# Kernel tuning notes

Measured on AMD Instinct MI355X. Metric: run time of the kernel, lower is better.

## Reference

```python
import jax, jax.numpy as jnp
import numpy as np

B, N, K, E, D, L, LM = 4, 5000, 4, 80000, 512, 6, 3
EPS_MSG = 1e-7   # GENConv message eps
EPS_SM = 1e-16   # PyG scatter-softmax eps
EPS_BN = 1e-5    # BatchNorm eps (eval: running mean=0, var=1)
EPS_LN = 1e-5


def setup_inputs() -> dict:
    key = jax.random.key(0)
    ks = jax.random.split(key, 12)
    s = 0.04  # weight scale for stability
    return {
        "x_idx": jax.random.randint(ks[0], (B, N, K), 0, 25, dtype=jnp.int32),
        "edge_index": jax.random.randint(ks[1], (2, E), 0, N, dtype=jnp.int32),
        "edge_weight": jax.random.uniform(ks[2], (E,), dtype=jnp.float32),
        "node_emb": jax.random.normal(ks[3], (25, D), dtype=jnp.float32),
        "W1": jax.random.normal(ks[4], (L, D, 2 * D), dtype=jnp.float32) * s,
        "b1": jnp.zeros((L, 2 * D), jnp.float32),
        "g1": jnp.ones((L, 2 * D), jnp.float32),
        "be1": jnp.zeros((L, 2 * D), jnp.float32),
        "W2": jax.random.normal(ks[5], (L, 2 * D, D), dtype=jnp.float32) * s,
        "b2": jnp.zeros((L, D), jnp.float32),
        "ln_g": jnp.ones((D,), jnp.float32),
        "ln_b": jnp.zeros((D,), jnp.float32),
        "Wm": jax.random.normal(ks[6], (LM, D, D), dtype=jnp.float32) * s,
        "bm": jnp.zeros((LM, D), jnp.float32),
        "Wout": jax.random.normal(ks[7], (D, 1), dtype=jnp.float32) * s,
        "bout": jnp.zeros((1,), jnp.float32),
    }


def _gen_conv(x, src, dst, edge_weight, W1, b1, g1, be1, W2, b2):
    # x: [B,N,D]; GENConv(aggr='softmax', t=1, num_layers=2, norm='batch' in eval)
    x_j = x[:, src, :]                                            # [B,E,D] gather
    msg = jax.nn.relu(x_j + edge_weight[None, :, None]) + EPS_MSG # [B,E,D]

    def seg_softmax_agg(m):  # m: [E,D] -> [N,D]
        mx = jax.ops.segment_max(m, dst, num_segments=N)          # [N,D]
        ex = jnp.exp(m - mx[dst])
        den = jax.ops.segment_sum(ex, dst, num_segments=N)
        alpha = ex / (den[dst] + EPS_SM)
        return jax.ops.segment_sum(m * alpha, dst, num_segments=N)

    agg = jax.vmap(seg_softmax_agg)(msg)                          # [B,N,D]
    out = agg + x                                                 # residual with x_dst
    h = out @ W1 + b1                                             # [B,N,2D]
    h = h / jnp.sqrt(1.0 + EPS_BN) * g1 + be1                     # BN eval (mean=0, var=1)
    h = jax.nn.relu(h)
    return h @ W2 + b2                                            # [B,N,D]


def reference(x_idx, edge_index, edge_weight, node_emb, W1, b1, g1, be1, W2, b2,
              ln_g, ln_b, Wm, bm, Wout, bout):
    src, dst = edge_index[0], edge_index[1]
    x = node_emb[x_idx].sum(axis=2)                               # [B,N,D]
    for l in range(W1.shape[0]):
        x = _gen_conv(x, src, dst, edge_weight,
                      W1[l], b1[l], g1[l], be1[l], W2[l], b2[l])
        x = jax.nn.relu(x)                                        # EncoderLayer relu (dropout=id in eval)
    mu = x.mean(axis=-1, keepdims=True)
    var = jnp.mean(jnp.square(x - mu), axis=-1, keepdims=True)
    h = (x - mu) * jax.lax.rsqrt(var + EPS_LN) * ln_g + ln_b      # LayerNorm
    for l in range(Wm.shape[0]):
        h = jax.nn.gelu(h @ Wm[l] + bm[l], approximate=False)
    out = h @ Wout + bout                                         # [B,N,1]
    return out.mean(axis=1)                                       # [B,1]
```

## Files before the change

kernel.cpp:

```cpp
#include <hip/hip_runtime.h>
#include <hip/hip_fp16.h>

#define BB 4
#define NN 5000
#define KK 4
#define EE 80000
#define DD 512
#define LL 6
#define LMM 3

typedef _Float16 f16x8 __attribute__((ext_vector_type(8)));
typedef _Float16 f16x4 __attribute__((ext_vector_type(4)));
typedef _Float16 f16x2 __attribute__((ext_vector_type(2)));
typedef float f32x4 __attribute__((ext_vector_type(4)));

__device__ __forceinline__ void async_copy16(_Float16* lds, const _Float16* g) {
    __builtin_amdgcn_global_load_lds((const __attribute__((address_space(1))) void*)g,
                                     (__attribute__((address_space(3))) void*)lds,
                                     16, 0, 0);
}

__global__ void zero_int2(int* a, int* b, int n) {
    int i = blockIdx.x * blockDim.x + threadIdx.x;
    if (i < n) { a[i] = 0; b[i] = 0; }
}

__global__ void count_deg(const int* __restrict__ dst, int* __restrict__ deg) {
    int e = blockIdx.x * blockDim.x + threadIdx.x;
    if (e < EE) atomicAdd(&deg[dst[e]], 1);
}

__global__ __launch_bounds__(1024) void scan_off(const int* __restrict__ deg, int* __restrict__ off) {
    __shared__ int s[1024];
    const int n = NN, tot = NN + 1;
    const int per = (tot + 1023) / 1024;
    int tid = threadIdx.x;
    int start = tid * per;
    int loc[8];
    int sum = 0;
    for (int i = 0; i < per; i++) {
        int idx = start + i;
        int v = (idx < n) ? deg[idx] : 0;
        loc[i] = sum; sum += v;
    }
    s[tid] = sum; __syncthreads();
    for (int o = 1; o < 1024; o <<= 1) {
        int v = (tid >= o) ? s[tid - o] : 0;
        __syncthreads();
        s[tid] += v;
        __syncthreads();
    }
    int base = (tid > 0) ? s[tid - 1] : 0;
    for (int i = 0; i < per; i++) {
        int idx = start + i;
        if (idx < tot) off[idx] = base + loc[i];
    }
}

__global__ void scatter_edges(const int* __restrict__ src, const int* __restrict__ dst,
                              const float* __restrict__ ew, const int* __restrict__ off,
                              int* __restrict__ cursor, int* __restrict__ srcs, float* __restrict__ wss) {
    int e = blockIdx.x * blockDim.x + threadIdx.x;
    if (e >= EE) return;
    int d = dst[e];
    int p = atomicAdd(&cursor[d], 1);
    int idx = off[d] + p;
    srcs[idx] = src[e];
    wss[idx] = ew[e];
}

__global__ __launch_bounds__(256) void embed_kernel(const int* __restrict__ x_idx,
                                                    const float* __restrict__ emb,
                                                    _Float16* __restrict__ x) {
    int row = blockIdx.x;
    int d = threadIdx.x * 2;
    int4 iv = *reinterpret_cast<const int4*>(x_idx + (size_t)row * 4);
    float2 a = *reinterpret_cast<const float2*>(emb + (size_t)iv.x * DD + d);
    float2 b = *reinterpret_cast<const float2*>(emb + (size_t)iv.y * DD + d);
    float2 c = *reinterpret_cast<const float2*>(emb + (size_t)iv.z * DD + d);
    float2 e = *reinterpret_cast<const float2*>(emb + (size_t)iv.w * DD + d);
    f16x2 v;
    v[0] = (_Float16)(a.x + b.x + c.x + e.x);
    v[1] = (_Float16)(a.y + b.y + c.y + e.y);
    *reinterpret_cast<f16x2*>(x + (size_t)row * DD + d) = v;
}

__global__ __launch_bounds__(128) void conv_kernel(const _Float16* __restrict__ x,
                                                   const int* __restrict__ srcs,
                                                   const float* __restrict__ wss,
                                                   const int* __restrict__ off,
                                                   _Float16* __restrict__ t) {
    int n = blockIdx.x, b = blockIdx.y, tid = threadIdx.x;
    const _Float16* xb = x + (size_t)b * NN * DD;
    int e0 = off[n], e1 = off[n + 1];
    __shared__ int   ss[64];
    __shared__ float sw[64];
    int d0 = tid * 4;
    float S0 = 0.f, S1 = 0.f, S2 = 0.f, S3 = 0.f;
    float Z0 = 0.f, Z1 = 0.f, Z2 = 0.f, Z3 = 0.f;
    for (int base = e0; base < e1; base += 64) {
        int cnt = min(64, e1 - base);
        if (tid < cnt) { ss[tid] = srcs[base + tid]; sw[tid] = wss[base + tid]; }
        __syncthreads();
        for (int j = 0; j < cnt; j++) {
            f16x4 xv = *reinterpret_cast<const f16x4*>(xb + (size_t)ss[j] * DD + d0);
            float w = sw[j];
            float m0 = fmaxf((float)xv[0] + w, 0.f) + 1e-7f;
            float m1 = fmaxf((float)xv[1] + w, 0.f) + 1e-7f;
            float m2 = fmaxf((float)xv[2] + w, 0.f) + 1e-7f;
            float m3 = fmaxf((float)xv[3] + w, 0.f) + 1e-7f;
            float p0 = __expf(m0), p1 = __expf(m1), p2 = __expf(m2), p3 = __expf(m3);
            S0 += p0; Z0 = fmaf(m0, p0, Z0);
            S1 += p1; Z1 = fmaf(m1, p1, Z1);
            S2 += p2; Z2 = fmaf(m2, p2, Z2);
            S3 += p3; Z3 = fmaf(m3, p3, Z3);
        }
        __syncthreads();
    }
    f16x4 xn = *reinterpret_cast<const f16x4*>(xb + (size_t)n * DD + d0);
    f16x4 o;
    o[0] = (_Float16)(Z0 / (S0 + 1e-16f) + (float)xn[0]);
    o[1] = (_Float16)(Z1 / (S1 + 1e-16f) + (float)xn[1]);
    o[2] = (_Float16)(Z2 / (S2 + 1e-16f) + (float)xn[2]);
    o[3] = (_Float16)(Z3 / (S3 + 1e-16f) + (float)xn[3]);
    *reinterpret_cast<f16x4*>(t + ((size_t)b * NN + n) * DD + d0) = o;
}

__global__ void transpose_f32_f16(const float* __restrict__ W, _Float16* __restrict__ Wt,
                                  int K, int Nc) {
    __shared__ float tile[32][33];
    size_t loff = (size_t)blockIdx.z * K * Nc;
    int n0 = blockIdx.x * 32, k0 = blockIdx.y * 32;
    int tx = threadIdx.x, ty = threadIdx.y;
    for (int i = 0; i < 32; i += 8)
        tile[ty + i][tx] = W[loff + (size_t)(k0 + ty + i) * Nc + n0 + tx];
    __syncthreads();
    for (int i = 0; i < 32; i += 8)
        Wt[loff + (size_t)(n0 + ty + i) * K + k0 + tx] = (_Float16)tile[tx][ty + i];
}

template <int MODE>
__global__ __launch_bounds__(256) void gemm_kernel(const _Float16* __restrict__ A,
                                                   const _Float16* __restrict__ Bt,
                                                   const float* __restrict__ bias,
                                                   const float* __restrict__ g,
                                                   const float* __restrict__ be,
                                                   _Float16* __restrict__ Cout,
                                                   int M, int N, int K, int nt) {
    constexpr int BM = 128, BN = 128, BK = 32;
    constexpr int BUF = (BM + BN) * BK;
    __shared__ __align__(16) _Float16 smem[2 * BUF];
    int tid = threadIdx.x;
    int bid = blockIdx.x;
    int m0 = (bid / nt) * BM, n0 = (bid % nt) * BN;
    int lane = tid & 63, wave = tid >> 6;
    int wm = (wave & 1) * 64, wn = (wave >> 1) * 64;
    int l16 = lane & 15, quad = lane >> 4;
    int r0 = tid >> 2, c0 = (tid & 3) * 8;
    int r1 = (tid + 256) >> 2, c1 = ((tid + 256) & 3) * 8;
    const _Float16* pa0 = A + (size_t)min(m0 + r0, M - 1) * K + c0;
    const _Float16* pa1 = A + (size_t)min(m0 + r1, M - 1) * K + c1;
    const _Float16* pb0 = Bt + (size_t)(n0 + r0) * K + c0;
    const _Float16* pb1 = Bt + (size_t)(n0 + r1) * K + c1;
    int la0 = tid * 8, la1 = (tid + 256) * 8;
    int lb0 = BM * BK + la0, lb1 = BM * BK + la1;

    f32x4 acc[4][4] = {};
    async_copy16(smem + la0, pa0);
    async_copy16(smem + la1, pa1);
    async_copy16(smem + lb0, pb0);
    async_copy16(smem + lb1, pb1);
    int buf = 0;
    for (int k0 = 0; k0 < K; k0 += BK, buf ^= BUF) {
        __syncthreads();
        int kn = k0 + BK;
        int nb = buf ^ BUF;
        if (kn < K) {
            async_copy16(smem + nb + la0, pa0 + kn);
            async_copy16(smem + nb + la1, pa1 + kn);
            async_copy16(smem + nb + lb0, pb0 + kn);
            async_copy16(smem + nb + lb1, pb1 + kn);
        }
        f16x8 af[4], bf[4];
#pragma unroll
        for (int i = 0; i < 4; i++)
            af[i] = *reinterpret_cast<const f16x8*>(&smem[buf + (wm + i * 16 + l16) * BK + quad * 8]);
#pragma unroll
        for (int j = 0; j < 4; j++)
            bf[j] = *reinterpret_cast<const f16x8*>(&smem[buf + BM * BK + (wn + j * 16 + l16) * BK + quad * 8]);
#pragma unroll
        for (int i = 0; i < 4; i++)
#pragma unroll
            for (int j = 0; j < 4; j++)
                acc[i][j] = __builtin_amdgcn_mfma_f32_16x16x32_f16(af[i], bf[j], acc[i][j], 0, 0, 0);
    }
    __syncthreads();
    const float invs = rsqrtf(1.0f + 1e-5f);
    _Float16* Ct = smem;
#pragma unroll
    for (int p = 0; p < 2; p++) {
        if ((wave >> 1) == p) {
#pragma unroll
            for (int i = 0; i < 4; i++) {
#pragma unroll
                for (int j = 0; j < 4; j++) {
                    int col = n0 + wn + j * 16 + l16;
#pragma unroll
                    for (int r = 0; r < 4; r++) {
                        float v = acc[i][j][r] + bias[col];
                        if (MODE == 0) {
                            v = fmaxf(v * (g[col] * invs) + be[col], 0.f);
                        } else if (MODE == 1) {
                            v = fmaxf(v, 0.f);
                        } else {
                            v = 0.5f * v * (1.0f + erff(v * 0.70710678118654752f));
                        }
                        Ct[(wm + i * 16 + quad * 4 + r) * 64 + j * 16 + l16] = (_Float16)v;
                    }
                }
            }
        }
        __syncthreads();
#pragma unroll
        for (int k = 0; k < 4; k++) {
            int ch = tid + 256 * k;
            int row = ch >> 3, cc = (ch & 7) * 8;
            int grow = m0 + row;
            if (grow < M)
                *reinterpret_cast<f16x8*>(Cout + (size_t)grow * N + n0 + p * 64 + cc) =
                    *reinterpret_cast<const f16x8*>(&Ct[row * 64 + cc]);
        }
        __syncthreads();
    }
}

__device__ __forceinline__ float block_sum_256(float v, volatile float* sbuf) {
    __syncthreads();
    for (int s = 32; s; s >>= 1) v += __shfl_down(v, s);
    int wv = threadIdx.x >> 6, ln = threadIdx.x & 63;
    if (ln == 0) sbuf[wv] = v;
    __syncthreads();
    if (threadIdx.x == 0) sbuf[4] = sbuf[0] + sbuf[1] + sbuf[2] + sbuf[3];
    __syncthreads();
    return sbuf[4];
}

__global__ __launch_bounds__(256) void ln_kernel(const _Float16* __restrict__ x,
                                                 const float* __restrict__ lg,
                                                 const float* __restrict__ lb,
                                                 _Float16* __restrict__ t) {
    __shared__ float sbuf[5];
    size_t row = blockIdx.x;
    int d = threadIdx.x * 2;
    f16x2 xv = *reinterpret_cast<const f16x2*>(x + row * DD + d);
    float v0 = (float)xv[0], v1 = (float)xv[1];
    float mu = block_sum_256(v0 + v1, sbuf) * (1.0f / DD);
    float d0 = v0 - mu, d1 = v1 - mu;
    float var = block_sum_256(d0 * d0 + d1 * d1, sbuf) * (1.0f / DD);
    float rs = rsqrtf(var + 1e-5f);
    f16x2 o;
    o[0] = (_Float16)(d0 * rs * lg[d] + lb[d]);
    o[1] = (_Float16)(d1 * rs * lg[d + 1] + lb[d + 1]);
    *reinterpret_cast<f16x2*>(t + row * DD + d) = o;
}

__global__ void init_out(float* out, const float* __restrict__ bout) {
    if (threadIdx.x < BB) out[threadIdx.x] = bout[0];
}

__global__ __launch_bounds__(256) void final_reduce(const _Float16* __restrict__ h,
                                                    const float* __restrict__ wout,
                                                    float* __restrict__ out) {
    int b = blockIdx.y;
    const _Float16* hb = h + (size_t)b * NN * DD;
    int lane = threadIdx.x & 63, wave = threadIdx.x >> 6;
    float wv[8];
#pragma unroll
    for (int j = 0; j < 8; j++) wv[j] = wout[lane * 8 + j];
    float acc = 0.f;
    for (int n = blockIdx.x * 4 + wave; n < NN; n += gridDim.x * 4) {
        f16x8 hv = *reinterpret_cast<const f16x8*>(hb + (size_t)n * DD + lane * 8);
#pragma unroll
        for (int j = 0; j < 8; j++) acc += (float)hv[j] * wv[j];
    }
    for (int s = 32; s; s >>= 1) acc += __shfl_down(acc, s);
    __shared__ float sb[4];
    if (lane == 0) sb[wave] = acc;
    __syncthreads();
    if (threadIdx.x == 0) atomicAdd(&out[b], (sb[0] + sb[1] + sb[2] + sb[3]) * (1.0f / NN));
}

extern "C" void kernel_launch(void* const* d_in, const int* in_sizes, int n_in,
                              void* d_out, int out_size, void* d_ws, size_t ws_size,
                              hipStream_t stream) {
    const int*   x_idx = (const int*)d_in[0];
    const int*   eidx  = (const int*)d_in[1];
    const float* ew    = (const float*)d_in[2];
    const float* emb   = (const float*)d_in[3];
    const float* W1    = (const float*)d_in[4];
    const float* b1    = (const float*)d_in[5];
    const float* g1    = (const float*)d_in[6];
    const float* be1   = (const float*)d_in[7];
    const float* W2    = (const float*)d_in[8];
    const float* b2    = (const float*)d_in[9];
    const float* lng   = (const float*)d_in[10];
    const float* lnb   = (const float*)d_in[11];
    const float* Wm    = (const float*)d_in[12];
    const float* bm    = (const float*)d_in[13];
    const float* Wout  = (const float*)d_in[14];
    const float* bout  = (const float*)d_in[15];
    float* out = (float*)d_out;

    char* w = (char*)d_ws;
    size_t o = 0;
    auto alloc = [&](size_t bytes) -> void* {
        void* p = w + o;
        o = (o + bytes + 255) & ~(size_t)255;
        return p;
    };
    _Float16*  x    = (_Float16*)alloc((size_t)BB * NN * DD * 2);
    _Float16*  t    = (_Float16*)alloc((size_t)BB * NN * DD * 2);
    _Float16*  h    = (_Float16*)alloc((size_t)BB * NN * 2 * DD * 2);
    _Float16*  W1t  = (_Float16*)alloc((size_t)LL * 2 * DD * DD * 2);
    _Float16*  W2t  = (_Float16*)alloc((size_t)LL * DD * 2 * DD * 2);
    _Float16*  Wmt  = (_Float16*)alloc((size_t)LMM * DD * DD * 2);
    int*    deg    = (int*)alloc((size_t)NN * 4);
    int*    offs   = (int*)alloc((size_t)(NN + 1) * 4);
    int*    cursor = (int*)alloc((size_t)NN * 4);
    int*    srcs   = (int*)alloc((size_t)EE * 4);
    float*  wss    = (float*)alloc((size_t)EE * 4);

    const int* src = eidx;
    const int* dst = eidx + EE;

    zero_int2<<<(NN + 255) / 256, 256, 0, stream>>>(deg, cursor, NN);
    count_deg<<<(EE + 255) / 256, 256, 0, stream>>>(dst, deg);
    scan_off<<<1, 1024, 0, stream>>>(deg, offs);
    scatter_edges<<<(EE + 255) / 256, 256, 0, stream>>>(src, dst, ew, offs, cursor, srcs, wss);
    embed_kernel<<<BB * NN, 256, 0, stream>>>(x_idx, emb, x);

    transpose_f32_f16<<<dim3(2 * DD / 32, DD / 32, LL), dim3(32, 8), 0, stream>>>(W1, W1t, DD, 2 * DD);
    transpose_f32_f16<<<dim3(DD / 32, 2 * DD / 32, LL), dim3(32, 8), 0, stream>>>(W2, W2t, 2 * DD, DD);
    transpose_f32_f16<<<dim3(DD / 32, DD / 32, LMM), dim3(32, 8), 0, stream>>>(Wm, Wmt, DD, DD);

    const int M = BB * NN;
    const int mt = (M + 127) / 128;
    for (int l = 0; l < LL; l++) {
        conv_kernel<<<dim3(NN, BB), 128, 0, stream>>>(x, srcs, wss, offs, t);
        gemm_kernel<0><<<mt * 8, 256, 0, stream>>>(
            t, W1t + (size_t)l * 2 * DD * DD, b1 + (size_t)l * 2 * DD,
            g1 + (size_t)l * 2 * DD, be1 + (size_t)l * 2 * DD, h, M, 2 * DD, DD, 8);
        gemm_kernel<1><<<mt * 4, 256, 0, stream>>>(
            h, W2t + (size_t)l * DD * 2 * DD, b2 + (size_t)l * DD,
            nullptr, nullptr, x, M, DD, 2 * DD, 4);
    }
    ln_kernel<<<M, 256, 0, stream>>>(x, lng, lnb, t);
    gemm_kernel<2><<<mt * 4, 256, 0, stream>>>(
        t, Wmt, bm, nullptr, nullptr, h, M, DD, DD, 4);
    gemm_kernel<2><<<mt * 4, 256, 0, stream>>>(
        h, Wmt + (size_t)DD * DD, bm + DD, nullptr, nullptr, t, M, DD, DD, 4);
    gemm_kernel<2><<<mt * 4, 256, 0, stream>>>(
        t, Wmt + (size_t)2 * DD * DD, bm + 2 * DD, nullptr, nullptr, h, M, DD, DD, 4);
    init_out<<<1, 64, 0, stream>>>(out, bout);
    final_reduce<<<dim3(32, BB), 256, 0, stream>>>(h, Wout, out);
}
```

Baseline: 1.002 ms.

## Use wave-per-node conv, swizzle GEMM LDS, and XCD-aware tile mapping

The message-aggregation kernel now assigns one 64-lane wave per destination node, with each lane handling 8 features. This drops block-wide barriers and widens gathers to 16-byte loads. The GEMM applies an XOR swizzle to LDS column chunks to reduce bank conflicts on fragment reads. It also remaps block IDs so consecutive row tiles land on the same XCD for L2 reuse of A/B, padding the row-tile count to a multiple of 8. The padding adds a few redundant tiles, and the epsilon handling in the softmax is rearranged algebraically.

```diff
diff --git a/kernel.cpp b/kernel.cpp
--- a/kernel.cpp
+++ b/kernel.cpp
@@ -10,7 +10,6 @@
 #define LMM 3
 
 typedef _Float16 f16x8 __attribute__((ext_vector_type(8)));
-typedef _Float16 f16x4 __attribute__((ext_vector_type(4)));
 typedef _Float16 f16x2 __attribute__((ext_vector_type(2)));
 typedef float f32x4 __attribute__((ext_vector_type(4)));
 
@@ -90,40 +89,39 @@
                                                    const float* __restrict__ wss,
                                                    const int* __restrict__ off,
                                                    _Float16* __restrict__ t) {
-    int n = blockIdx.x, b = blockIdx.y, tid = threadIdx.x;
+    int b = blockIdx.x;
+    int wave = threadIdx.x >> 6, lane = threadIdx.x & 63;
+    int n = blockIdx.y * 2 + wave;
     const _Float16* xb = x + (size_t)b * NN * DD;
     int e0 = off[n], e1 = off[n + 1];
-    __shared__ int   ss[64];
-    __shared__ float sw[64];
-    int d0 = tid * 4;
-    float S0 = 0.f, S1 = 0.f, S2 = 0.f, S3 = 0.f;
-    float Z0 = 0.f, Z1 = 0.f, Z2 = 0.f, Z3 = 0.f;
+    __shared__ int   ss[2][64];
+    __shared__ float sw[2][64];
+    int d0 = lane * 8;
+    float S[8] = {0.f, 0.f, 0.f, 0.f, 0.f, 0.f, 0.f, 0.f};
+    float Z[8] = {0.f, 0.f, 0.f, 0.f, 0.f, 0.f, 0.f, 0.f};
     for (int base = e0; base < e1; base += 64) {
         int cnt = min(64, e1 - base);
-        if (tid < cnt) { ss[tid] = srcs[base + tid]; sw[tid] = wss[base + tid]; }
-        __syncthreads();
+        if (lane < cnt) { ss[wave][lane] = srcs[base + lane]; sw[wave][lane] = wss[base + lane]; }
         for (int j = 0; j < cnt; j++) {
-            f16x4 xv = *reinterpret_cast<const f16x4*>(xb + (size_t)ss[j] * DD + d0);
-            float w = sw[j];
-            float m0 = fmaxf((float)xv[0] + w, 0.f) + 1e-7f;
-            float m1 = fmaxf((float)xv[1] + w, 0.f) + 1e-7f;
-            float m2 = fmaxf((float)xv[2] + w, 0.f) + 1e-7f;
-            float m3 = fmaxf((float)xv[3] + w, 0.f) + 1e-7f;
-            float p0 = __expf(m0), p1 = __expf(m1), p2 = __expf(m2), p3 = __expf(m3);
-            S0 += p0; Z0 = fmaf(m0, p0, Z0);
-            S1 += p1; Z1 = fmaf(m1, p1, Z1);
-            S2 += p2; Z2 = fmaf(m2, p2, Z2);
-            S3 += p3; Z3 = fmaf(m3, p3, Z3);
+            f16x8 xv = *reinterpret_cast<const f16x8*>(xb + (size_t)ss[wave][j] * DD + d0);
+            float w = sw[wave][j];
+#pragma unroll
+            for (int q = 0; q < 8; q++) {
+                float m = fmaxf((float)xv[q] + w, 0.f);
+                float p = __expf(m);
+                S[q] += p;
+                Z[q] = fmaf(m, p, Z[q]);
+            }
         }
-        __syncthreads();
-    }
-    f16x4 xn = *reinterpret_cast<const f16x4*>(xb + (size_t)n * DD + d0);
-    f16x4 o;
-    o[0] = (_Float16)(Z0 / (S0 + 1e-16f) + (float)xn[0]);
-    o[1] = (_Float16)(Z1 / (S1 + 1e-16f) + (float)xn[1]);
-    o[2] = (_Float16)(Z2 / (S2 + 1e-16f) + (float)xn[2]);
-    o[3] = (_Float16)(Z3 / (S3 + 1e-16f) + (float)xn[3]);
-    *reinterpret_cast<f16x4*>(t + ((size_t)b * NN + n) * DD + d0) = o;
+    }
+    f16x8 xn = *reinterpret_cast<const f16x8*>(xb + (size_t)n * DD + d0);
+    f16x8 o;
+#pragma unroll
+    for (int q = 0; q < 8; q++) {
+        float agg = (e1 > e0) ? (Z[q] / (S[q] + 1e-16f) + 1e-7f) : 0.f;
+        o[q] = (_Float16)(agg + (float)xn[q]);
+    }
+    *reinterpret_cast<f16x8*>(t + ((size_t)b * NN + n) * DD + d0) = o;
 }
 
 __global__ void transpose_f32_f16(const float* __restrict__ W, _Float16* __restrict__ Wt,
@@ -152,16 +150,19 @@
     __shared__ __align__(16) _Float16 smem[2 * BUF];
     int tid = threadIdx.x;
     int bid = blockIdx.x;
-    int m0 = (bid / nt) * BM, n0 = (bid % nt) * BN;
+    int xcd = bid & 7, gidx = bid >> 3;
+    int m0 = (xcd + 8 * (gidx / nt)) * BM;
+    int n0 = (gidx % nt) * BN;
     int lane = tid & 63, wave = tid >> 6;
     int wm = (wave & 1) * 64, wn = (wave >> 1) * 64;
     int l16 = lane & 15, quad = lane >> 4;
-    int r0 = tid >> 2, c0 = (tid & 3) * 8;
-    int r1 = (tid + 256) >> 2, c1 = ((tid + 256) & 3) * 8;
-    const _Float16* pa0 = A + (size_t)min(m0 + r0, M - 1) * K + c0;
-    const _Float16* pa1 = A + (size_t)min(m0 + r1, M - 1) * K + c1;
-    const _Float16* pb0 = Bt + (size_t)(n0 + r0) * K + c0;
-    const _Float16* pb1 = Bt + (size_t)(n0 + r1) * K + c1;
+    int r0 = tid >> 2, r1 = r0 + 64;
+    int c0s = ((tid & 3) ^ (r0 & 3)) * 8;
+    int c1s = ((tid & 3) ^ (r1 & 3)) * 8;
+    const _Float16* pa0 = A + (size_t)min(m0 + r0, M - 1) * K + c0s;
+    const _Float16* pa1 = A + (size_t)min(m0 + r1, M - 1) * K + c1s;
+    const _Float16* pb0 = Bt + (size_t)(n0 + r0) * K + c0s;
+    const _Float16* pb1 = Bt + (size_t)(n0 + r1) * K + c1s;
     int la0 = tid * 8, la1 = (tid + 256) * 8;
     int lb0 = BM * BK + la0, lb1 = BM * BK + la1;
 
@@ -171,6 +172,7 @@
     async_copy16(smem + lb0, pb0);
     async_copy16(smem + lb1, pb1);
     int buf = 0;
+    int qa = (quad ^ (l16 & 3)) * 8;
     for (int k0 = 0; k0 < K; k0 += BK, buf ^= BUF) {
         __syncthreads();
         int kn = k0 + BK;
@@ -184,10 +186,10 @@
         f16x8 af[4], bf[4];
 #pragma unroll
         for (int i = 0; i < 4; i++)
-            af[i] = *reinterpret_cast<const f16x8*>(&smem[buf + (wm + i * 16 + l16) * BK + quad * 8]);
+            af[i] = *reinterpret_cast<const f16x8*>(&smem[buf + (wm + i * 16 + l16) * BK + qa]);
 #pragma unroll
         for (int j = 0; j < 4; j++)
-            bf[j] = *reinterpret_cast<const f16x8*>(&smem[buf + BM * BK + (wn + j * 16 + l16) * BK + quad * 8]);
+            bf[j] = *reinterpret_cast<const f16x8*>(&smem[buf + BM * BK + (wn + j * 16 + l16) * BK + qa]);
 #pragma unroll
         for (int i = 0; i < 4; i++)
 #pragma unroll
@@ -344,22 +346,22 @@
     transpose_f32_f16<<<dim3(DD / 32, DD / 32, LMM), dim3(32, 8), 0, stream>>>(Wm, Wmt, DD, DD);
 
     const int M = BB * NN;
-    const int mt = (M + 127) / 128;
+    const int mt8 = ((M + 127) / 128 + 7) & ~7;
     for (int l = 0; l < LL; l++) {
-        conv_kernel<<<dim3(NN, BB), 128, 0, stream>>>(x, srcs, wss, offs, t);
-        gemm_kernel<0><<<mt * 8, 256, 0, stream>>>(
+        conv_kernel<<<dim3(BB, NN / 2), 128, 0, stream>>>(x, srcs, wss, offs, t);
+        gemm_kernel<0><<<mt8 * 8, 256, 0, stream>>>(
             t, W1t + (size_t)l * 2 * DD * DD, b1 + (size_t)l * 2 * DD,
             g1 + (size_t)l * 2 * DD, be1 + (size_t)l * 2 * DD, h, M, 2 * DD, DD, 8);
-        gemm_kernel<1><<<mt * 4, 256, 0, stream>>>(
+        gemm_kernel<1><<<mt8 * 4, 256, 0, stream>>>(
             h, W2t + (size_t)l * DD * 2 * DD, b2 + (size_t)l * DD,
             nullptr, nullptr, x, M, DD, 2 * DD, 4);
     }
     ln_kernel<<<M, 256, 0, stream>>>(x, lng, lnb, t);
-    gemm_kernel<2><<<mt * 4, 256, 0, stream>>>(
+    gemm_kernel<2><<<mt8 * 4, 256, 0, stream>>>(
         t, Wmt, bm, nullptr, nullptr, h, M, DD, DD, 4);
-    gemm_kernel<2><<<mt * 4, 256, 0, stream>>>(
+    gemm_kernel<2><<<mt8 * 4, 256, 0, stream>>>(
         h, Wmt + (size_t)DD * DD, bm + DD, nullptr, nullptr, t, M, DD, DD, 4);
-    gemm_kernel<2><<<mt * 4, 256, 0, stream>>>(
+    gemm_kernel<2><<<mt8 * 4, 256, 0, stream>>>(
         t, Wmt + (size_t)2 * DD * DD, bm + 2 * DD, nullptr, nullptr, h, M, DD, DD, 4);
     init_out<<<1, 64, 0, stream>>>(out, bout);
     final_reduce<<<dim3(32, BB), 256, 0, stream>>>(h, Wout, out);
```

After: 933.7 us. -6.8%, faster.
